# Performance work log

Hardware: AMD Instinct MI355X
Metric: run time of the kernel (lower is better)

## Reference

```python
import jax, jax.numpy as jnp
import numpy as np

B, N, D = 16, 1024, 16  # graphs, nodes, embedding_dim


def setup_inputs() -> dict:
    key = jax.random.key(0)
    ks = jax.random.split(key, 13)
    s = 0.05  # small weight scale to keep exp(alpha) well-behaved
    return {
        "X": jax.random.normal(ks[0], (B, N, D), dtype=jnp.float32),
        "init_param": jax.random.normal(ks[1], (2,), dtype=jnp.float32) * s,
        "Wq": jax.random.normal(ks[2], (D - 1, D, D), dtype=jnp.float32) * s,
        "bq": jax.random.normal(ks[3], (D - 1, D), dtype=jnp.float32) * s,
        "Wk": jax.random.normal(ks[4], (D - 1, D, D), dtype=jnp.float32) * s,
        "bk": jax.random.normal(ks[5], (D - 1, D), dtype=jnp.float32) * s,
        "Wv": jax.random.normal(ks[6], (D - 1, D, D), dtype=jnp.float32) * s,
        "bv": jax.random.normal(ks[7], (D - 1, D), dtype=jnp.float32) * s,
        "Wo": jax.random.normal(ks[8], (D - 1, D, D), dtype=jnp.float32) * s,
        "bo": jax.random.normal(ks[9], (D - 1, D), dtype=jnp.float32) * s,
        "Wf": jax.random.normal(ks[10], (D - 1, 2, D), dtype=jnp.float32) * s,
        "bf": jax.random.normal(ks[11], (D - 1, 2), dtype=jnp.float32) * s,
    }


def reference(X, init_param, Wq, bq, Wk, bk, Wv, bv, Wo, bo, Wf, bf):
    b, n, d = X.shape
    dt = X.dtype
    Zs = []
    logdet = jnp.zeros((b, n), dt)
    for i in range(d):
        if i == 0:
            mu, alpha = init_param[0], init_param[1]
        else:
            l = i - 1
            Xi = X[:, :, :i]  # [B,N,i] growing ragged slice
            Q = Xi @ Wq[l, :i, :i].T + bq[l, :i]
            K = Xi @ Wk[l, :i, :i].T + bk[l, :i]
            V = Xi @ Wv[l, :i, :i].T + bv[l, :i]
            # SAB/MAB: softmax(QK^T / sqrt(dim_V=i)); num_heads=1
            A = jax.nn.softmax(
                jnp.einsum("bnd,bmd->bnm", Q, K) / jnp.sqrt(jnp.asarray(i, dt)),
                axis=-1,
            )  # [B,N,N]
            O = Q + jnp.einsum("bnm,bmd->bnd", A, V)
            O = O + jax.nn.relu(O @ Wo[l, :i, :i].T + bo[l, :i])
            out = O @ Wf[l, :, :i].T + bf[l]  # [B,N,2]
            mu, alpha = out[..., 0], out[..., 1]
        Zs.append((X[:, :, i] - mu) / jnp.exp(alpha))
        logdet = logdet - alpha
    Z = jnp.stack(Zs, axis=-1)
    return Z, logdet
```

## Files before the change

kernel.cpp:

```cpp
#include <hip/hip_runtime.h>
#include <math.h>

#define Bb 16
#define Nn 1024
#define Dd 16
#define NL 15

typedef __attribute__((ext_vector_type(8))) short short8;
typedef __attribute__((ext_vector_type(4))) float f32x4;
typedef __attribute__((ext_vector_type(16))) float f32x16;
typedef __attribute__((ext_vector_type(4))) unsigned uint4v;

#if __has_builtin(__builtin_amdgcn_exp2f)
#define EXP2(x) __builtin_amdgcn_exp2f(x)
#else
#define EXP2(x) exp2f(x)
#endif

#define VSTR 1044
#define V_OFF 32768
#define RS_OFF 65536
#define LDS_TOTAL 69632

__device__ __forceinline__ unsigned pack2bf(float a, float b) {
    unsigned ua = __float_as_uint(a) + 0x8000u;
    unsigned ub = __float_as_uint(b) + 0x8000u;
    return (ua >> 16) | (ub & 0xffff0000u);
}
__device__ __forceinline__ unsigned short bf1(float a) {
    return (unsigned short)((__float_as_uint(a) + 0x8000u) >> 16);
}

__device__ __forceinline__ void project(const float* __restrict__ xrow,
                                        const float* __restrict__ W,
                                        const float* __restrict__ bias,
                                        int i, float* __restrict__ q) {
#pragma unroll
    for (int r = 0; r < 16; r++) q[r] = 0.f;
    for (int c = 0; c < i; c++) {
        float xc = xrow[c];
#pragma unroll
        for (int r = 0; r < 16; r++) q[r] = fmaf(xc, W[r * 16 + c], q[r]);
    }
#pragma unroll
    for (int r = 0; r < 16; r++) q[r] = (r < i) ? (q[r] + bias[r]) : 0.f;
}

__device__ __forceinline__ void load_row16(const float* __restrict__ p, float* __restrict__ x) {
    const float4* xp = (const float4*)p;
    float4 a = xp[0], b = xp[1], c = xp[2], d = xp[3];
    x[0]=a.x; x[1]=a.y; x[2]=a.z; x[3]=a.w;
    x[4]=b.x; x[5]=b.y; x[6]=b.z; x[7]=b.w;
    x[8]=c.x; x[9]=c.y; x[10]=c.z; x[11]=c.w;
    x[12]=d.x; x[13]=d.y; x[14]=d.z; x[15]=d.w;
}

__launch_bounds__(1024, 4)
__global__ void gf_fused(const float* __restrict__ X,
                         const float* __restrict__ Wq, const float* __restrict__ bq,
                         const float* __restrict__ Wk, const float* __restrict__ bk,
                         const float* __restrict__ Wv, const float* __restrict__ bv,
                         const float* __restrict__ Wo, const float* __restrict__ bo,
                         const float* __restrict__ Wf, const float* __restrict__ bf,
                         float* __restrict__ als, float* __restrict__ out) {
    extern __shared__ char smem[];
    const int l = blockIdx.x, b = blockIdx.y, i = l + 1;
    const int t = threadIdx.x;
    const int wid = t >> 6, lane = t & 63;
    const int q31 = lane & 31, h = lane >> 5;
    const float qscale = 1.4426950408889634f * rsqrtf((float)i);

    unsigned short* Ksh = (unsigned short*)smem;
    unsigned short* Vsh = (unsigned short*)(smem + V_OFF);

    const float* Xb  = X  + (size_t)b * Nn * Dd;
    const float* wq  = Wq + l * 256;  const float* bql = bq + l * 16;
    const float* wk  = Wk + l * 256;  const float* bkl = bk + l * 16;
    const float* wvp = Wv + l * 256;  const float* bvl = bv + l * 16;
    const float* wo  = Wo + l * 256;  const float* bol = bo + l * 16;
    const float* wf  = Wf + l * 32;   const float* bfl = bf + l * 2;

    unsigned qu[8];
    {
        float xr[16]; load_row16(Xb + (size_t)t * Dd, xr);
        float tmp[16];
        unsigned u[8];

        project(xr, wk, bkl, i, tmp);
#pragma unroll
        for (int r = 0; r < 8; r++) u[r] = pack2bf(tmp[2*r], tmp[2*r+1]);
        {
            uint4* kd = (uint4*)(Ksh + t * 16);
            kd[0] = make_uint4(u[0], u[1], u[2], u[3]);
            kd[1] = make_uint4(u[4], u[5], u[6], u[7]);
        }

        project(xr, wvp, bvl, i, tmp);
#pragma unroll
        for (int d = 0; d < 16; d++) Vsh[d * VSTR + t] = bf1(tmp[d]);

        project(xr, wq, bql, i, tmp);
#pragma unroll
        for (int r = 0; r < 8; r++) qu[r] = pack2bf(tmp[2*r] * qscale, tmp[2*r+1] * qscale);
    }
    __syncthreads();

    short8 qf0, qf1;
    {
        unsigned d0[4], d1[4];
#pragma unroll
        for (int j = 0; j < 4; j++) {
            unsigned lo = __shfl(qu[j], q31);
            unsigned hi = __shfl(qu[4 + j], q31);
            d0[j] = h ? hi : lo;
            lo = __shfl(qu[j], 32 + q31);
            hi = __shfl(qu[4 + j], 32 + q31);
            d1[j] = h ? hi : lo;
        }
        uint4v v0 = {d0[0], d0[1], d0[2], d0[3]};
        uint4v v1 = {d1[0], d1[1], d1[2], d1[3]};
        qf0 = __builtin_bit_cast(short8, v0);
        qf1 = __builtin_bit_cast(short8, v1);
    }

    f32x16 zf16 = {};
    f32x16 D0 = {}, D1 = {};
    float rs0 = 0.f, rs1 = 0.f;

    const unsigned short* Kp   = Ksh + (size_t)q31 * 16 + h * 8;
    const unsigned short* Vrow = Vsh + (size_t)(q31 & 15) * VSTR;

    short8 kf = *(const short8*)Kp;

    for (int kb = 0; kb < Nn; kb += 32) {
        short8 kfn = *(const short8*)(Kp + (size_t)((kb + 32) & (Nn - 1)) * 16);

        f32x16 s0 = __builtin_amdgcn_mfma_f32_32x32x16_bf16(kf, qf0, zf16, 0, 0, 0);
        f32x16 s1 = __builtin_amdgcn_mfma_f32_32x32x16_bf16(kf, qf1, zf16, 0, 0, 0);
        kf = kfn;

        unsigned p0[8], p1[8];
#pragma unroll
        for (int g = 0; g < 4; g++) {
            float e0 = EXP2(s0[4*g+0]), e1 = EXP2(s0[4*g+1]);
            float e2 = EXP2(s0[4*g+2]), e3 = EXP2(s0[4*g+3]);
            rs0 += (e0 + e1) + (e2 + e3);
            p0[2*g]   = pack2bf(e0, e1);
            p0[2*g+1] = pack2bf(e2, e3);
        }
#pragma unroll
        for (int g = 0; g < 4; g++) {
            float e0 = EXP2(s1[4*g+0]), e1 = EXP2(s1[4*g+1]);
            float e2 = EXP2(s1[4*g+2]), e3 = EXP2(s1[4*g+3]);
            rs1 += (e0 + e1) + (e2 + e3);
            p1[2*g]   = pack2bf(e0, e1);
            p1[2*g+1] = pack2bf(e2, e3);
        }

#pragma unroll
        for (int s = 0; s < 2; s++) {
            const unsigned short* vb = Vrow + kb + 16*s + 4*h;
            uint2 va = *(const uint2*)vb;
            uint2 vc = *(const uint2*)(vb + 8);
            uint4v vv = {va.x, va.y, vc.x, vc.y};
            short8 vf = __builtin_bit_cast(short8, vv);
            uint4v a0 = {p0[4*s], p0[4*s+1], p0[4*s+2], p0[4*s+3]};
            uint4v a1 = {p1[4*s], p1[4*s+1], p1[4*s+2], p1[4*s+3]};
            D0 = __builtin_amdgcn_mfma_f32_32x32x16_bf16(__builtin_bit_cast(short8, a0), vf, D0, 0, 0, 0);
            D1 = __builtin_amdgcn_mfma_f32_32x32x16_bf16(__builtin_bit_cast(short8, a1), vf, D1, 0, 0, 0);
        }
    }

    rs0 += __shfl_xor(rs0, 32);
    rs1 += __shfl_xor(rs1, 32);

    __syncthreads();

    float* Ow = (float*)smem + wid * 1024;
    if (q31 < 16) {
#pragma unroll
        for (int r = 0; r < 16; r++) {
            int m = (r & 3) + 8 * (r >> 2) + 4 * h;
            Ow[m * 16 + q31]        = D0[r];
            Ow[(m + 32) * 16 + q31] = D1[r];
        }
    }
    float* Rw = (float*)(smem + RS_OFF) + wid * 64;
    if (h == 0) { Rw[q31] = rs0; Rw[32 + q31] = rs1; }

    {
        float xr[16]; load_row16(Xb + (size_t)t * Dd, xr);
        float q[16];  project(xr, wq, bql, i, q);
        const float* orow = (const float*)smem + wid * 1024 + lane * 16;
        const float  inv  = 1.f / Rw[lane];

        float a[16];
#pragma unroll
        for (int c = 0; c < 16; c++) a[c] = q[c] + orow[c] * inv;

        float tt[16];
#pragma unroll
        for (int r = 0; r < 16; r++) {
            float acc = bol[r];
#pragma unroll
            for (int c = 0; c < 16; c++) acc = fmaf(a[c], wo[r * 16 + c], acc);
            tt[r] = fmaxf(acc, 0.f);
        }
#pragma unroll
        for (int r = 0; r < 16; r++) a[r] += (r < i) ? tt[r] : 0.f;

        float mu = bfl[0], al = bfl[1];
#pragma unroll
        for (int c = 0; c < 16; c++) {
            mu = fmaf(a[c], wf[c], mu);
            al = fmaf(a[c], wf[16 + c], al);
        }
        out[((size_t)(b * Nn + t)) * Dd + i] = (xr[i] - mu) * __expf(-al);
        als[(size_t)l * (Bb * Nn) + b * Nn + t] = al;
    }
}

__launch_bounds__(1024)
__global__ void gf_final(const float* __restrict__ X, const float* __restrict__ ip,
                         const float* __restrict__ als, float* __restrict__ out) {
    const int idx = blockIdx.x * 1024 + threadIdx.x;
    const float mu = ip[0], a0 = ip[1];
    float x0 = X[(size_t)idx * Dd];
    out[(size_t)idx * Dd] = (x0 - mu) * __expf(-a0);
    float ld = -a0;
#pragma unroll
    for (int l = 0; l < NL; l++) ld -= als[(size_t)l * (Bb * Nn) + idx];
    out[(size_t)Bb * Nn * Dd + idx] = ld;
}

__global__ void gf_init(const float* __restrict__ X, const float* __restrict__ ip,
                        float* __restrict__ out) {
    int idx = blockIdx.x * blockDim.x + threadIdx.x;
    if (idx >= Bb * Nn) return;
    float mu = ip[0], alpha = ip[1];
    float x0 = X[(size_t)idx * Dd];
    out[(size_t)idx * Dd] = (x0 - mu) * __expf(-alpha);
    out[(size_t)Bb * Nn * Dd + idx] = -alpha;
}

__launch_bounds__(512, 2)
__global__ void gf_layer_fb(const float* __restrict__ X,
                            const float* __restrict__ Wq, const float* __restrict__ bq,
                            const float* __restrict__ Wk, const float* __restrict__ bk,
                            const float* __restrict__ Wv, const float* __restrict__ bv,
                            const float* __restrict__ Wo, const float* __restrict__ bo,
                            const float* __restrict__ Wf, const float* __restrict__ bf,
                            float* __restrict__ out) {
    const int l = blockIdx.x, b = blockIdx.y, i = l + 1, t = threadIdx.x;
    const float rscale = rsqrtf((float)i);
    __shared__ float Ksh[512 * 16];
    __shared__ float Vsh[512 * 16];
    const float* Xb = X + (size_t)b * Nn * Dd;
    const float* wq = Wq + l * 256; const float* wk = Wk + l * 256;
    const float* wv = Wv + l * 256; const float* wo = Wo + l * 256;
    const float* wf = Wf + l * 32;
    const float* bql = bq + l * 16; const float* bkl = bk + l * 16;
    const float* bvl = bv + l * 16; const float* bol = bo + l * 16;
    const float* bfl = bf + l * 2;
    const int n0 = t, n1 = t + 512;
    float q0[16], q1[16], xi0, xi1;
    {
        float xr[16];
        load_row16(Xb + (size_t)n0 * Dd, xr); xi0 = xr[i]; project(xr, wq, bql, i, q0);
        load_row16(Xb + (size_t)n1 * Dd, xr); xi1 = xr[i]; project(xr, wq, bql, i, q1);
    }
    float o0[16], o1[16];
#pragma unroll
    for (int c = 0; c < 16; c++) { o0[c] = 0.f; o1[c] = 0.f; }
    float ls0 = 0.f, ls1 = 0.f;
    for (int ch = 0; ch < 2; ch++) {
        float kr[16], vr[16];
        {
            float kx[16];
            load_row16(Xb + (size_t)(ch * 512 + t) * Dd, kx);
            project(kx, wk, bkl, i, kr);
            project(kx, wv, bvl, i, vr);
        }
        __syncthreads();
#pragma unroll
        for (int j = 0; j < 4; j++) {
            ((float4*)&Ksh[t * 16])[j] = ((float4*)kr)[j];
            ((float4*)&Vsh[t * 16])[j] = ((float4*)vr)[j];
        }
        __syncthreads();
        for (int k = 0; k < 512; k++) {
            float kk[16], vv[16];
#pragma unroll
            for (int j = 0; j < 4; j++) ((float4*)kk)[j] = ((const float4*)&Ksh[k * 16])[j];
            float s0 = 0.f, s1 = 0.f;
#pragma unroll
            for (int c = 0; c < 16; c++) { s0 = fmaf(q0[c], kk[c], s0); s1 = fmaf(q1[c], kk[c], s1); }
            float p0 = __expf(s0 * rscale), p1 = __expf(s1 * rscale);
            ls0 += p0; ls1 += p1;
#pragma unroll
            for (int j = 0; j < 4; j++) ((float4*)vv)[j] = ((const float4*)&Vsh[k * 16])[j];
#pragma unroll
            for (int c = 0; c < 16; c++) { o0[c] = fmaf(p0, vv[c], o0[c]); o1[c] = fmaf(p1, vv[c], o1[c]); }
        }
        __syncthreads();
    }
    float* logdet = out + (size_t)Bb * Nn * Dd;
#pragma unroll
    for (int rowsel = 0; rowsel < 2; rowsel++) {
        const float* qr = rowsel ? q1 : q0; const float* orr = rowsel ? o1 : o0;
        float lsum = rowsel ? ls1 : ls0; float xin = rowsel ? xi1 : xi0;
        int n = rowsel ? n1 : n0;
        float a[16]; float inv = 1.f / lsum;
#pragma unroll
        for (int c = 0; c < 16; c++) a[c] = qr[c] + orr[c] * inv;
        float tt[16];
#pragma unroll
        for (int r = 0; r < 16; r++) {
            float acc = bol[r];
#pragma unroll
            for (int c = 0; c < 16; c++) acc = fmaf(a[c], wo[r * 16 + c], acc);
            tt[r] = fmaxf(acc, 0.f);
        }
#pragma unroll
        for (int r = 0; r < 16; r++) a[r] += (r < i) ? tt[r] : 0.f;
        float mu = bfl[0], al = bfl[1];
#pragma unroll
        for (int c = 0; c < 16; c++) { mu = fmaf(a[c], wf[c], mu); al = fmaf(a[c], wf[16 + c], al); }
        out[((size_t)(b * Nn + n)) * Dd + i] = (xin - mu) * __expf(-al);
        atomicAdd(logdet + b * Nn + n, -al);
    }
}

extern "C" void kernel_launch(void* const* d_in, const int* in_sizes, int n_in,
                              void* d_out, int out_size, void* d_ws, size_t ws_size,
                              hipStream_t stream) {
    const float* X  = (const float*)d_in[0];
    const float* ip = (const float*)d_in[1];
    const float* Wq = (const float*)d_in[2];
    const float* bq = (const float*)d_in[3];
    const float* Wk = (const float*)d_in[4];
    const float* bk = (const float*)d_in[5];
    const float* Wv = (const float*)d_in[6];
    const float* bv = (const float*)d_in[7];
    const float* Wo = (const float*)d_in[8];
    const float* bo = (const float*)d_in[9];
    const float* Wf = (const float*)d_in[10];
    const float* bf = (const float*)d_in[11];
    float* out = (float*)d_out;

    const size_t need = (size_t)NL * Bb * Nn * sizeof(float);
    hipError_t e = hipFuncSetAttribute((const void*)gf_fused,
                                       hipFuncAttributeMaxDynamicSharedMemorySize,
                                       LDS_TOTAL);
    if (e == hipSuccess && ws_size >= need) {
        float* als = (float*)d_ws;
        gf_fused<<<dim3(NL, Bb), 1024, LDS_TOTAL, stream>>>(
            X, Wq, bq, Wk, bk, Wv, bv, Wo, bo, Wf, bf, als, out);
        gf_final<<<Bb, 1024, 0, stream>>>(X, ip, als, out);
    } else {
        gf_init<<<(Bb * Nn + 255) / 256, 256, 0, stream>>>(X, ip, out);
        gf_layer_fb<<<dim3(NL, Bb), 512, 0, stream>>>(
            X, Wq, bq, Wk, bk, Wv, bv, Wo, bo, Wf, bf, out);
    }
}
```

Measured before the change: 155.5 us.

## Split query rows across two blocks per layer-graph to double grid parallelism

Adds a third grid dimension so that each (layer, graph) pair is handled by two blocks, each owning 512 query rows. Both blocks still project the full K and V into LDS, but each wave now does one score MFMA per key tile instead of two. The grid grows from 240 to 480 blocks to fill more CUs, at the cost of computing K/V twice and leaving half the threads idle in the epilogue. The final kernel is also relaunched with 256-thread blocks so it spreads across more CUs.

```diff
diff --git a/kernel.cpp b/kernel.cpp
--- a/kernel.cpp
+++ b/kernel.cpp
@@ -7,7 +7,6 @@
 #define NL 15
 
 typedef __attribute__((ext_vector_type(8))) short short8;
-typedef __attribute__((ext_vector_type(4))) float f32x4;
 typedef __attribute__((ext_vector_type(16))) float f32x16;
 typedef __attribute__((ext_vector_type(4))) unsigned uint4v;
 
@@ -19,8 +18,8 @@
 
 #define VSTR 1044
 #define V_OFF 32768
-#define RS_OFF 65536
-#define LDS_TOTAL 69632
+#define RS_OFF 66176
+#define LDS_TOTAL 68224
 
 __device__ __forceinline__ unsigned pack2bf(float a, float b) {
     unsigned ua = __float_as_uint(a) + 0x8000u;
@@ -64,10 +63,11 @@
                          const float* __restrict__ Wf, const float* __restrict__ bf,
                          float* __restrict__ als, float* __restrict__ out) {
     extern __shared__ char smem[];
-    const int l = blockIdx.x, b = blockIdx.y, i = l + 1;
+    const int l = blockIdx.x, b = blockIdx.y, s = blockIdx.z, i = l + 1;
     const int t = threadIdx.x;
     const int wid = t >> 6, lane = t & 63;
     const int q31 = lane & 31, h = lane >> 5;
+    const int qbase = s * 512;
     const float qscale = 1.4426950408889634f * rsqrtf((float)i);
 
     unsigned short* Ksh = (unsigned short*)smem;
@@ -99,33 +99,30 @@
 #pragma unroll
         for (int d = 0; d < 16; d++) Vsh[d * VSTR + t] = bf1(tmp[d]);
 
-        project(xr, wq, bql, i, tmp);
+        const int qrow = qbase + wid * 32 + q31;
+        float xq[16]; load_row16(Xb + (size_t)qrow * Dd, xq);
+        project(xq, wq, bql, i, tmp);
 #pragma unroll
         for (int r = 0; r < 8; r++) qu[r] = pack2bf(tmp[2*r] * qscale, tmp[2*r+1] * qscale);
     }
     __syncthreads();
 
-    short8 qf0, qf1;
+    short8 qf;
     {
-        unsigned d0[4], d1[4];
+        unsigned d0[4];
 #pragma unroll
         for (int j = 0; j < 4; j++) {
             unsigned lo = __shfl(qu[j], q31);
             unsigned hi = __shfl(qu[4 + j], q31);
             d0[j] = h ? hi : lo;
-            lo = __shfl(qu[j], 32 + q31);
-            hi = __shfl(qu[4 + j], 32 + q31);
-            d1[j] = h ? hi : lo;
         }
         uint4v v0 = {d0[0], d0[1], d0[2], d0[3]};
-        uint4v v1 = {d1[0], d1[1], d1[2], d1[3]};
-        qf0 = __builtin_bit_cast(short8, v0);
-        qf1 = __builtin_bit_cast(short8, v1);
+        qf = __builtin_bit_cast(short8, v0);
     }
 
     f32x16 zf16 = {};
-    f32x16 D0 = {}, D1 = {};
-    float rs0 = 0.f, rs1 = 0.f;
+    f32x16 D0 = {};
+    float rs0 = 0.f;
 
     const unsigned short* Kp   = Ksh + (size_t)q31 * 16 + h * 8;
     const unsigned short* Vrow = Vsh + (size_t)(q31 & 15) * VSTR;
@@ -135,64 +132,71 @@
     for (int kb = 0; kb < Nn; kb += 32) {
         short8 kfn = *(const short8*)(Kp + (size_t)((kb + 32) & (Nn - 1)) * 16);
 
-        f32x16 s0 = __builtin_amdgcn_mfma_f32_32x32x16_bf16(kf, qf0, zf16, 0, 0, 0);
-        f32x16 s1 = __builtin_amdgcn_mfma_f32_32x32x16_bf16(kf, qf1, zf16, 0, 0, 0);
+        f32x16 s0 = __builtin_amdgcn_mfma_f32_32x32x16_bf16(kf, qf, zf16, 0, 0, 0);
         kf = kfn;
 
-        unsigned p0[8], p1[8];
-#pragma unroll
-        for (int g = 0; g < 4; g++) {
-            float e0 = EXP2(s0[4*g+0]), e1 = EXP2(s0[4*g+1]);
-            float e2 = EXP2(s0[4*g+2]), e3 = EXP2(s0[4*g+3]);
-            rs0 += (e0 + e1) + (e2 + e3);
-            p0[2*g]   = pack2bf(e0, e1);
-            p0[2*g+1] = pack2bf(e2, e3);
-        }
-#pragma unroll
-        for (int g = 0; g < 4; g++) {
-            float e0 = EXP2(s1[4*g+0]), e1 = EXP2(s1[4*g+1]);
-            float e2 = EXP2(s1[4*g+2]), e3 = EXP2(s1[4*g+3]);
-            rs1 += (e0 + e1) + (e2 + e3);
-            p1[2*g]   = pack2bf(e0, e1);
-            p1[2*g+1] = pack2bf(e2, e3);
-        }
-
-#pragma unroll
-        for (int s = 0; s < 2; s++) {
-            const unsigned short* vb = Vrow + kb + 16*s + 4*h;
+        {
+            unsigned pa[4];
+#pragma unroll
+            for (int g = 0; g < 2; g++) {
+                float e0 = EXP2(s0[4*g+0]), e1 = EXP2(s0[4*g+1]);
+                float e2 = EXP2(s0[4*g+2]), e3 = EXP2(s0[4*g+3]);
+                rs0 += (e0 + e1) + (e2 + e3);
+                pa[2*g]   = pack2bf(e0, e1);
+                pa[2*g+1] = pack2bf(e2, e3);
+            }
+            const unsigned short* vb = Vrow + kb + 4*h;
             uint2 va = *(const uint2*)vb;
             uint2 vc = *(const uint2*)(vb + 8);
             uint4v vv = {va.x, va.y, vc.x, vc.y};
-            short8 vf = __builtin_bit_cast(short8, vv);
-            uint4v a0 = {p0[4*s], p0[4*s+1], p0[4*s+2], p0[4*s+3]};
-            uint4v a1 = {p1[4*s], p1[4*s+1], p1[4*s+2], p1[4*s+3]};
-            D0 = __builtin_amdgcn_mfma_f32_32x32x16_bf16(__builtin_bit_cast(short8, a0), vf, D0, 0, 0, 0);
-            D1 = __builtin_amdgcn_mfma_f32_32x32x16_bf16(__builtin_bit_cast(short8, a1), vf, D1, 0, 0, 0);
+            uint4v a0 = {pa[0], pa[1], pa[2], pa[3]};
+            D0 = __builtin_amdgcn_mfma_f32_32x32x16_bf16(
+                     __builtin_bit_cast(short8, a0),
+                     __builtin_bit_cast(short8, vv), D0, 0, 0, 0);
+        }
+        {
+            unsigned pb[4];
+#pragma unroll
+            for (int g = 2; g < 4; g++) {
+                float e0 = EXP2(s0[4*g+0]), e1 = EXP2(s0[4*g+1]);
+                float e2 = EXP2(s0[4*g+2]), e3 = EXP2(s0[4*g+3]);
+                rs0 += (e0 + e1) + (e2 + e3);
+                pb[2*(g-2)]   = pack2bf(e0, e1);
+                pb[2*(g-2)+1] = pack2bf(e2, e3);
+            }
+            const unsigned short* vb = Vrow + kb + 16 + 4*h;
+            uint2 va = *(const uint2*)vb;
+            uint2 vc = *(const uint2*)(vb + 8);
+            uint4v vv = {va.x, va.y, vc.x, vc.y};
+            uint4v a0 = {pb[0], pb[1], pb[2], pb[3]};
+            D0 = __builtin_amdgcn_mfma_f32_32x32x16_bf16(
+                     __builtin_bit_cast(short8, a0),
+                     __builtin_bit_cast(short8, vv), D0, 0, 0, 0);
         }
     }
 
     rs0 += __shfl_xor(rs0, 32);
-    rs1 += __shfl_xor(rs1, 32);
 
     __syncthreads();
 
-    float* Ow = (float*)smem + wid * 1024;
+    float* Ow = (float*)smem;
     if (q31 < 16) {
 #pragma unroll
         for (int r = 0; r < 16; r++) {
             int m = (r & 3) + 8 * (r >> 2) + 4 * h;
-            Ow[m * 16 + q31]        = D0[r];
-            Ow[(m + 32) * 16 + q31] = D1[r];
-        }
-    }
-    float* Rw = (float*)(smem + RS_OFF) + wid * 64;
-    if (h == 0) { Rw[q31] = rs0; Rw[32 + q31] = rs1; }
-
-    {
-        float xr[16]; load_row16(Xb + (size_t)t * Dd, xr);
+            Ow[(wid * 32 + m) * 16 + q31] = D0[r];
+        }
+    }
+    float* Rw = (float*)(smem + RS_OFF);
+    if (h == 0) Rw[wid * 32 + q31] = rs0;
+    __syncthreads();
+
+    if (t < 512) {
+        const int n = qbase + t;
+        float xr[16]; load_row16(Xb + (size_t)n * Dd, xr);
         float q[16];  project(xr, wq, bql, i, q);
-        const float* orow = (const float*)smem + wid * 1024 + lane * 16;
-        const float  inv  = 1.f / Rw[lane];
+        const float* orow = Ow + t * 16;
+        const float  inv  = 1.f / Rw[t];
 
         float a[16];
 #pragma unroll
@@ -215,15 +219,15 @@
             mu = fmaf(a[c], wf[c], mu);
             al = fmaf(a[c], wf[16 + c], al);
         }
-        out[((size_t)(b * Nn + t)) * Dd + i] = (xr[i] - mu) * __expf(-al);
-        als[(size_t)l * (Bb * Nn) + b * Nn + t] = al;
-    }
-}
-
-__launch_bounds__(1024)
+        out[((size_t)(b * Nn + n)) * Dd + i] = (xr[i] - mu) * __expf(-al);
+        als[(size_t)l * (Bb * Nn) + b * Nn + n] = al;
+    }
+}
+
+__launch_bounds__(256)
 __global__ void gf_final(const float* __restrict__ X, const float* __restrict__ ip,
                          const float* __restrict__ als, float* __restrict__ out) {
-    const int idx = blockIdx.x * 1024 + threadIdx.x;
+    const int idx = blockIdx.x * 256 + threadIdx.x;
     const float mu = ip[0], a0 = ip[1];
     float x0 = X[(size_t)idx * Dd];
     out[(size_t)idx * Dd] = (x0 - mu) * __expf(-a0);
@@ -354,9 +358,9 @@
                                        LDS_TOTAL);
     if (e == hipSuccess && ws_size >= need) {
         float* als = (float*)d_ws;
-        gf_fused<<<dim3(NL, Bb), 1024, LDS_TOTAL, stream>>>(
+        gf_fused<<<dim3(NL, Bb, 2), 1024, LDS_TOTAL, stream>>>(
             X, Wq, bq, Wk, bk, Wv, bv, Wo, bo, Wf, bf, als, out);
-        gf_final<<<Bb, 1024, 0, stream>>>(X, ip, als, out);
+        gf_final<<<Bb * Nn / 256, 256, 0, stream>>>(X, ip, als, out);
     } else {
         gf_init<<<(Bb * Nn + 255) / 256, 256, 0, stream>>>(X, ip, out);
         gf_layer_fb<<<dim3(NL, Bb), 512, 0, stream>>>(
```

Result: slower. 174.7 us (+12.4%).

## Fold softmax row sums into MFMA via ones column, prefetch V, atomic logdet

Applied to the files above, without the earlier changes.

Lanes 16-31 of the P·V MFMA, which were padding, now read a row of bf16 ones, so the softmax denominators come out of the matrix unit instead of scalar exp-sum adds. V fragments are prefetched one iteration ahead like K, and exp results are packed with a byte-permute instead of shifts. The O staging buffer is padded to stride 17 to reduce LDS bank conflicts. The per-layer alpha workspace and the final reduction kernel are replaced by an init kernel plus atomicAdd of -alpha into logdet. This costs extra LDS and nondeterministic summation order.

```diff
diff --git a/kernel.cpp b/kernel.cpp
--- a/kernel.cpp
+++ b/kernel.cpp
@@ -7,7 +7,6 @@
 #define NL 15
 
 typedef __attribute__((ext_vector_type(8))) short short8;
-typedef __attribute__((ext_vector_type(4))) float f32x4;
 typedef __attribute__((ext_vector_type(16))) float f32x16;
 typedef __attribute__((ext_vector_type(4))) unsigned uint4v;
 
@@ -19,8 +18,9 @@
 
 #define VSTR 1044
 #define V_OFF 32768
-#define RS_OFF 65536
-#define LDS_TOTAL 69632
+#define RS_OFF 69632
+#define ONES_OFF 73728
+#define LDS_TOTAL 75776
 
 __device__ __forceinline__ unsigned pack2bf(float a, float b) {
     unsigned ua = __float_as_uint(a) + 0x8000u;
@@ -29,6 +29,16 @@
 }
 __device__ __forceinline__ unsigned short bf1(float a) {
     return (unsigned short)((__float_as_uint(a) + 0x8000u) >> 16);
+}
+
+__device__ __forceinline__ unsigned expperm(float x, float y) {
+    unsigned ex = __float_as_uint(EXP2(x));
+    unsigned ey = __float_as_uint(EXP2(y));
+#if __has_builtin(__builtin_amdgcn_perm)
+    return __builtin_amdgcn_perm(ey, ex, 0x07060302);
+#else
+    return (ex >> 16) | (ey & 0xffff0000u);
+#endif
 }
 
 __device__ __forceinline__ void project(const float* __restrict__ xrow,
@@ -55,182 +65,11 @@
     x[12]=d.x; x[13]=d.y; x[14]=d.z; x[15]=d.w;
 }
 
-__launch_bounds__(1024, 4)
-__global__ void gf_fused(const float* __restrict__ X,
-                         const float* __restrict__ Wq, const float* __restrict__ bq,
-                         const float* __restrict__ Wk, const float* __restrict__ bk,
-                         const float* __restrict__ Wv, const float* __restrict__ bv,
-                         const float* __restrict__ Wo, const float* __restrict__ bo,
-                         const float* __restrict__ Wf, const float* __restrict__ bf,
-                         float* __restrict__ als, float* __restrict__ out) {
-    extern __shared__ char smem[];
-    const int l = blockIdx.x, b = blockIdx.y, i = l + 1;
-    const int t = threadIdx.x;
-    const int wid = t >> 6, lane = t & 63;
-    const int q31 = lane & 31, h = lane >> 5;
-    const float qscale = 1.4426950408889634f * rsqrtf((float)i);
-
-    unsigned short* Ksh = (unsigned short*)smem;
-    unsigned short* Vsh = (unsigned short*)(smem + V_OFF);
-
-    const float* Xb  = X  + (size_t)b * Nn * Dd;
-    const float* wq  = Wq + l * 256;  const float* bql = bq + l * 16;
-    const float* wk  = Wk + l * 256;  const float* bkl = bk + l * 16;
-    const float* wvp = Wv + l * 256;  const float* bvl = bv + l * 16;
-    const float* wo  = Wo + l * 256;  const float* bol = bo + l * 16;
-    const float* wf  = Wf + l * 32;   const float* bfl = bf + l * 2;
-
-    unsigned qu[8];
-    {
-        float xr[16]; load_row16(Xb + (size_t)t * Dd, xr);
-        float tmp[16];
-        unsigned u[8];
-
-        project(xr, wk, bkl, i, tmp);
-#pragma unroll
-        for (int r = 0; r < 8; r++) u[r] = pack2bf(tmp[2*r], tmp[2*r+1]);
-        {
-            uint4* kd = (uint4*)(Ksh + t * 16);
-            kd[0] = make_uint4(u[0], u[1], u[2], u[3]);
-            kd[1] = make_uint4(u[4], u[5], u[6], u[7]);
-        }
-
-        project(xr, wvp, bvl, i, tmp);
-#pragma unroll
-        for (int d = 0; d < 16; d++) Vsh[d * VSTR + t] = bf1(tmp[d]);
-
-        project(xr, wq, bql, i, tmp);
-#pragma unroll
-        for (int r = 0; r < 8; r++) qu[r] = pack2bf(tmp[2*r] * qscale, tmp[2*r+1] * qscale);
-    }
-    __syncthreads();
-
-    short8 qf0, qf1;
-    {
-        unsigned d0[4], d1[4];
-#pragma unroll
-        for (int j = 0; j < 4; j++) {
-            unsigned lo = __shfl(qu[j], q31);
-            unsigned hi = __shfl(qu[4 + j], q31);
-            d0[j] = h ? hi : lo;
-            lo = __shfl(qu[j], 32 + q31);
-            hi = __shfl(qu[4 + j], 32 + q31);
-            d1[j] = h ? hi : lo;
-        }
-        uint4v v0 = {d0[0], d0[1], d0[2], d0[3]};
-        uint4v v1 = {d1[0], d1[1], d1[2], d1[3]};
-        qf0 = __builtin_bit_cast(short8, v0);
-        qf1 = __builtin_bit_cast(short8, v1);
-    }
-
-    f32x16 zf16 = {};
-    f32x16 D0 = {}, D1 = {};
-    float rs0 = 0.f, rs1 = 0.f;
-
-    const unsigned short* Kp   = Ksh + (size_t)q31 * 16 + h * 8;
-    const unsigned short* Vrow = Vsh + (size_t)(q31 & 15) * VSTR;
-
-    short8 kf = *(const short8*)Kp;
-
-    for (int kb = 0; kb < Nn; kb += 32) {
-        short8 kfn = *(const short8*)(Kp + (size_t)((kb + 32) & (Nn - 1)) * 16);
-
-        f32x16 s0 = __builtin_amdgcn_mfma_f32_32x32x16_bf16(kf, qf0, zf16, 0, 0, 0);
-        f32x16 s1 = __builtin_amdgcn_mfma_f32_32x32x16_bf16(kf, qf1, zf16, 0, 0, 0);
-        kf = kfn;
-
-        unsigned p0[8], p1[8];
-#pragma unroll
-        for (int g = 0; g < 4; g++) {
-            float e0 = EXP2(s0[4*g+0]), e1 = EXP2(s0[4*g+1]);
-            float e2 = EXP2(s0[4*g+2]), e3 = EXP2(s0[4*g+3]);
-            rs0 += (e0 + e1) + (e2 + e3);
-            p0[2*g]   = pack2bf(e0, e1);
-            p0[2*g+1] = pack2bf(e2, e3);
-        }
-#pragma unroll
-        for (int g = 0; g < 4; g++) {
-            float e0 = EXP2(s1[4*g+0]), e1 = EXP2(s1[4*g+1]);
-            float e2 = EXP2(s1[4*g+2]), e3 = EXP2(s1[4*g+3]);
-            rs1 += (e0 + e1) + (e2 + e3);
-            p1[2*g]   = pack2bf(e0, e1);
-            p1[2*g+1] = pack2bf(e2, e3);
-        }
-
-#pragma unroll
-        for (int s = 0; s < 2; s++) {
-            const unsigned short* vb = Vrow + kb + 16*s + 4*h;
-            uint2 va = *(const uint2*)vb;
-            uint2 vc = *(const uint2*)(vb + 8);
-            uint4v vv = {va.x, va.y, vc.x, vc.y};
-            short8 vf = __builtin_bit_cast(short8, vv);
-            uint4v a0 = {p0[4*s], p0[4*s+1], p0[4*s+2], p0[4*s+3]};
-            uint4v a1 = {p1[4*s], p1[4*s+1], p1[4*s+2], p1[4*s+3]};
-            D0 = __builtin_amdgcn_mfma_f32_32x32x16_bf16(__builtin_bit_cast(short8, a0), vf, D0, 0, 0, 0);
-            D1 = __builtin_amdgcn_mfma_f32_32x32x16_bf16(__builtin_bit_cast(short8, a1), vf, D1, 0, 0, 0);
-        }
-    }
-
-    rs0 += __shfl_xor(rs0, 32);
-    rs1 += __shfl_xor(rs1, 32);
-
-    __syncthreads();
-
-    float* Ow = (float*)smem + wid * 1024;
-    if (q31 < 16) {
-#pragma unroll
-        for (int r = 0; r < 16; r++) {
-            int m = (r & 3) + 8 * (r >> 2) + 4 * h;
-            Ow[m * 16 + q31]        = D0[r];
-            Ow[(m + 32) * 16 + q31] = D1[r];
-        }
-    }
-    float* Rw = (float*)(smem + RS_OFF) + wid * 64;
-    if (h == 0) { Rw[q31] = rs0; Rw[32 + q31] = rs1; }
-
-    {
-        float xr[16]; load_row16(Xb + (size_t)t * Dd, xr);
-        float q[16];  project(xr, wq, bql, i, q);
-        const float* orow = (const float*)smem + wid * 1024 + lane * 16;
-        const float  inv  = 1.f / Rw[lane];
-
-        float a[16];
-#pragma unroll
-        for (int c = 0; c < 16; c++) a[c] = q[c] + orow[c] * inv;
-
-        float tt[16];
-#pragma unroll
-        for (int r = 0; r < 16; r++) {
-            float acc = bol[r];
-#pragma unroll
-            for (int c = 0; c < 16; c++) acc = fmaf(a[c], wo[r * 16 + c], acc);
-            tt[r] = fmaxf(acc, 0.f);
-        }
-#pragma unroll
-        for (int r = 0; r < 16; r++) a[r] += (r < i) ? tt[r] : 0.f;
-
-        float mu = bfl[0], al = bfl[1];
-#pragma unroll
-        for (int c = 0; c < 16; c++) {
-            mu = fmaf(a[c], wf[c], mu);
-            al = fmaf(a[c], wf[16 + c], al);
-        }
-        out[((size_t)(b * Nn + t)) * Dd + i] = (xr[i] - mu) * __expf(-al);
-        als[(size_t)l * (Bb * Nn) + b * Nn + t] = al;
-    }
-}
-
-__launch_bounds__(1024)
-__global__ void gf_final(const float* __restrict__ X, const float* __restrict__ ip,
-                         const float* __restrict__ als, float* __restrict__ out) {
-    const int idx = blockIdx.x * 1024 + threadIdx.x;
-    const float mu = ip[0], a0 = ip[1];
-    float x0 = X[(size_t)idx * Dd];
-    out[(size_t)idx * Dd] = (x0 - mu) * __expf(-a0);
-    float ld = -a0;
-#pragma unroll
-    for (int l = 0; l < NL; l++) ld -= als[(size_t)l * (Bb * Nn) + idx];
-    out[(size_t)Bb * Nn * Dd + idx] = ld;
+__device__ __forceinline__ short8 ldv(const unsigned short* __restrict__ p) {
+    uint2 a = *(const uint2*)p;
+    uint2 b = *(const uint2*)(p + 8);
+    uint4v v = {a.x, a.y, b.x, b.y};
+    return __builtin_bit_cast(short8, v);
 }
 
 __global__ void gf_init(const float* __restrict__ X, const float* __restrict__ ip,
@@ -241,6 +80,173 @@
     float x0 = X[(size_t)idx * Dd];
     out[(size_t)idx * Dd] = (x0 - mu) * __expf(-alpha);
     out[(size_t)Bb * Nn * Dd + idx] = -alpha;
+}
+
+__launch_bounds__(1024, 4)
+__global__ void gf_fused(const float* __restrict__ X,
+                         const float* __restrict__ Wq, const float* __restrict__ bq,
+                         const float* __restrict__ Wk, const float* __restrict__ bk,
+                         const float* __restrict__ Wv, const float* __restrict__ bv,
+                         const float* __restrict__ Wo, const float* __restrict__ bo,
+                         const float* __restrict__ Wf, const float* __restrict__ bf,
+                         float* __restrict__ out) {
+    extern __shared__ char smem[];
+    const int l = blockIdx.x, b = blockIdx.y, i = l + 1;
+    const int t = threadIdx.x;
+    const int wid = t >> 6, lane = t & 63;
+    const int q31 = lane & 31, h = lane >> 5;
+    const float qscale = 1.4426950408889634f * rsqrtf((float)i);
+
+    unsigned short* Ksh  = (unsigned short*)smem;
+    unsigned short* Vsh  = (unsigned short*)(smem + V_OFF);
+    unsigned short* Ones = (unsigned short*)(smem + ONES_OFF);
+
+    const float* Xb  = X  + (size_t)b * Nn * Dd;
+    const float* wq  = Wq + l * 256;  const float* bql = bq + l * 16;
+    const float* wk  = Wk + l * 256;  const float* bkl = bk + l * 16;
+    const float* wvp = Wv + l * 256;  const float* bvl = bv + l * 16;
+    const float* wo  = Wo + l * 256;  const float* bol = bo + l * 16;
+    const float* wf  = Wf + l * 32;   const float* bfl = bf + l * 2;
+
+    unsigned qu[8];
+    {
+        float xr[16]; load_row16(Xb + (size_t)t * Dd, xr);
+        float tmp[16];
+        unsigned u[8];
+
+        project(xr, wk, bkl, i, tmp);
+#pragma unroll
+        for (int r = 0; r < 8; r++) u[r] = pack2bf(tmp[2*r], tmp[2*r+1]);
+        {
+            uint4* kd = (uint4*)(Ksh + t * 16);
+            kd[0] = make_uint4(u[0], u[1], u[2], u[3]);
+            kd[1] = make_uint4(u[4], u[5], u[6], u[7]);
+        }
+
+        project(xr, wvp, bvl, i, tmp);
+#pragma unroll
+        for (int d = 0; d < 16; d++) Vsh[d * VSTR + t] = bf1(tmp[d]);
+
+        Ones[t] = 0x3F80;
+
+        project(xr, wq, bql, i, tmp);
+#pragma unroll
+        for (int r = 0; r < 8; r++) qu[r] = pack2bf(tmp[2*r] * qscale, tmp[2*r+1] * qscale);
+    }
+    __syncthreads();
+
+    short8 qf0, qf1;
+    {
+        unsigned d0[4], d1[4];
+#pragma unroll
+        for (int j = 0; j < 4; j++) {
+            unsigned lo = __shfl(qu[j], q31);
+            unsigned hi = __shfl(qu[4 + j], q31);
+            d0[j] = h ? hi : lo;
+            lo = __shfl(qu[j], 32 + q31);
+            hi = __shfl(qu[4 + j], 32 + q31);
+            d1[j] = h ? hi : lo;
+        }
+        uint4v v0 = {d0[0], d0[1], d0[2], d0[3]};
+        uint4v v1 = {d1[0], d1[1], d1[2], d1[3]};
+        qf0 = __builtin_bit_cast(short8, v0);
+        qf1 = __builtin_bit_cast(short8, v1);
+    }
+
+    f32x16 zf16 = {};
+    f32x16 D0 = {}, D1 = {};
+
+    const unsigned short* Kp = Ksh + (size_t)q31 * 16 + h * 8;
+    const unsigned short* Vp = ((q31 < 16) ? (Vsh + (size_t)q31 * VSTR) : Ones) + 4 * h;
+
+    short8 kf  = *(const short8*)Kp;
+    short8 vc0 = ldv(Vp);
+    short8 vc1 = ldv(Vp + 16);
+
+    for (int kb = 0; kb < Nn; kb += 32) {
+        const int kn = (kb + 32) & (Nn - 1);
+        short8 kfn = *(const short8*)(Kp + (size_t)kn * 16);
+        short8 vn0 = ldv(Vp + kn);
+        short8 vn1 = ldv(Vp + kn + 16);
+
+        f32x16 s0 = __builtin_amdgcn_mfma_f32_32x32x16_bf16(kf, qf0, zf16, 0, 0, 0);
+        f32x16 s1 = __builtin_amdgcn_mfma_f32_32x32x16_bf16(kf, qf1, zf16, 0, 0, 0);
+        kf = kfn;
+
+        {
+            uint4v a0 = {expperm(s0[0], s0[1]), expperm(s0[2], s0[3]),
+                         expperm(s0[4], s0[5]), expperm(s0[6], s0[7])};
+            D0 = __builtin_amdgcn_mfma_f32_32x32x16_bf16(
+                     __builtin_bit_cast(short8, a0), vc0, D0, 0, 0, 0);
+            uint4v a1 = {expperm(s1[0], s1[1]), expperm(s1[2], s1[3]),
+                         expperm(s1[4], s1[5]), expperm(s1[6], s1[7])};
+            D1 = __builtin_amdgcn_mfma_f32_32x32x16_bf16(
+                     __builtin_bit_cast(short8, a1), vc0, D1, 0, 0, 0);
+        }
+        {
+            uint4v a0 = {expperm(s0[8], s0[9]),  expperm(s0[10], s0[11]),
+                         expperm(s0[12], s0[13]), expperm(s0[14], s0[15])};
+            D0 = __builtin_amdgcn_mfma_f32_32x32x16_bf16(
+                     __builtin_bit_cast(short8, a0), vc1, D0, 0, 0, 0);
+            uint4v a1 = {expperm(s1[8], s1[9]),  expperm(s1[10], s1[11]),
+                         expperm(s1[12], s1[13]), expperm(s1[14], s1[15])};
+            D1 = __builtin_amdgcn_mfma_f32_32x32x16_bf16(
+                     __builtin_bit_cast(short8, a1), vc1, D1, 0, 0, 0);
+        }
+        vc0 = vn0; vc1 = vn1;
+    }
+
+    __syncthreads();
+
+    float* Ow = (float*)smem + wid * (64 * 17);
+    if (q31 < 16) {
+#pragma unroll
+        for (int r = 0; r < 16; r++) {
+            int m = (r & 3) + 8 * (r >> 2) + 4 * h;
+            Ow[m * 17 + q31]        = D0[r];
+            Ow[(m + 32) * 17 + q31] = D1[r];
+        }
+    }
+    float* Rw = (float*)(smem + RS_OFF) + wid * 64;
+    if (q31 == 16) {
+#pragma unroll
+        for (int r = 0; r < 16; r++) {
+            int m = (r & 3) + 8 * (r >> 2) + 4 * h;
+            Rw[m]      = D0[r];
+            Rw[32 + m] = D1[r];
+        }
+    }
+
+    {
+        float xr[16]; load_row16(Xb + (size_t)t * Dd, xr);
+        float q[16];  project(xr, wq, bql, i, q);
+        const float* orow = (const float*)smem + wid * (64 * 17) + lane * 17;
+        const float  inv  = 1.f / Rw[lane];
+
+        float a[16];
+#pragma unroll
+        for (int c = 0; c < 16; c++) a[c] = q[c] + orow[c] * inv;
+
+        float tt[16];
+#pragma unroll
+        for (int r = 0; r < 16; r++) {
+            float acc = bol[r];
+#pragma unroll
+            for (int c = 0; c < 16; c++) acc = fmaf(a[c], wo[r * 16 + c], acc);
+            tt[r] = fmaxf(acc, 0.f);
+        }
+#pragma unroll
+        for (int r = 0; r < 16; r++) a[r] += (r < i) ? tt[r] : 0.f;
+
+        float mu = bfl[0], al = bfl[1];
+#pragma unroll
+        for (int c = 0; c < 16; c++) {
+            mu = fmaf(a[c], wf[c], mu);
+            al = fmaf(a[c], wf[16 + c], al);
+        }
+        out[((size_t)(b * Nn + t)) * Dd + i] = (xr[i] - mu) * __expf(-al);
+        atomicAdd(out + (size_t)Bb * Nn * Dd + b * Nn + t, -al);
+    }
 }
 
 __launch_bounds__(512, 2)
@@ -348,17 +354,15 @@
     const float* bf = (const float*)d_in[11];
     float* out = (float*)d_out;
 
-    const size_t need = (size_t)NL * Bb * Nn * sizeof(float);
+    gf_init<<<(Bb * Nn + 255) / 256, 256, 0, stream>>>(X, ip, out);
+
     hipError_t e = hipFuncSetAttribute((const void*)gf_fused,
                                        hipFuncAttributeMaxDynamicSharedMemorySize,
                                        LDS_TOTAL);
-    if (e == hipSuccess && ws_size >= need) {
-        float* als = (float*)d_ws;
+    if (e == hipSuccess) {
         gf_fused<<<dim3(NL, Bb), 1024, LDS_TOTAL, stream>>>(
-            X, Wq, bq, Wk, bk, Wv, bv, Wo, bo, Wf, bf, als, out);
-        gf_final<<<Bb, 1024, 0, stream>>>(X, ip, als, out);
+            X, Wq, bq, Wk, bk, Wv, bv, Wo, bo, Wf, bf, out);
     } else {
-        gf_init<<<(Bb * Nn + 255) / 256, 256, 0, stream>>>(X, ip, out);
         gf_layer_fb<<<dim3(NL, Bb), 512, 0, stream>>>(
             X, Wq, bq, Wk, bk, Wv, bv, Wo, bo, Wf, bf, out);
     }
```

Result: faster. 140.7 us (-9.5%).
